# Optimization experiments

Measured on AMD Instinct MI355X. Metric: run time of the kernel, lower is better.

## Reference

```python
import jax, jax.numpy as jnp
import numpy as np

L = 10  # lattice_size


def _wilson_plaquette_loop(field, x):
    # Faithful translation of compute_wilson_loop: product of exp(plaquette) over 6 (mu,nu) pairs.
    coords = x[0, :4].astype(jnp.int32) % L
    loop = jnp.ones((1,), dtype=field.dtype)
    for mu in range(4):
        for nu in range(mu + 1, 4):
            pos = coords
            link1 = field[pos[0], pos[1], pos[2], mu]
            pos = pos.at[mu].set((pos[mu] + 1) % L)
            link2 = field[pos[0], pos[1], pos[2], nu]
            pos = pos.at[nu].set((pos[nu] + 1) % L)
            link3 = -field[pos[0], pos[1], pos[2], mu]
            pos = pos.at[mu].add(-1)  # original has no mod here
            link4 = -field[coords[0], coords[1], coords[2], nu]
            loop = loop * jnp.exp(link1 + link2 + link3 - (-link4) + 0.0 if False else link1 + link2 + link3 + link4)
    return loop


def setup_inputs() -> dict:
    key = jax.random.key(0)
    ks = jax.random.split(key, 20)
    s = 0.02  # scale weights to keep activations numerically sane
    d = jnp.float32
    return {
        'x': jax.random.normal(ks[0], (16384, 4), d),
        'field': jax.random.normal(ks[1], (L, L, L, 4), d),
        'fw1': jax.random.normal(ks[2], (4, 2048), d) * s,
        'fb1': jax.random.normal(ks[3], (2048,), d) * s,
        'fw2': jax.random.normal(ks[4], (2048, 4096), d) * s,
        'fb2': jax.random.normal(ks[5], (4096,), d) * s,
        'ww1': jax.random.normal(ks[6], (4096, 2048), d) * s,
        'wb1': jax.random.normal(ks[7], (2048,), d) * s,
        'ww2': jax.random.normal(ks[8], (2048, 1024), d) * s,
        'wb2': jax.random.normal(ks[9], (1024,), d) * s,
        'ww3': jax.random.normal(ks[10], (1024, 1), d) * s,
        'wb3': jax.random.normal(ks[11], (1,), d) * s,
        'tw1': jax.random.normal(ks[12], (4096, 2048), d) * s,
        'tb1': jax.random.normal(ks[13], (2048,), d) * s,
        'tw2': jax.random.normal(ks[14], (2048, 1), d) * s,
        'tb2': jax.random.normal(ks[15], (1,), d) * s,
    }


def reference(x, field, fw1, fb1, fw2, fb2, ww1, wb1, ww2, wb2, ww3, wb3, tw1, tb1, tw2, tb2):
    x4 = x[:, :4]
    h = jnp.maximum(x4 @ fw1 + fb1, 0.0)
    field_output = h @ fw2 + fb2                       # [B, dim]
    plaq = _wilson_plaquette_loop(field, x4)           # [1] (computed in torch forward, not returned)
    w = jnp.maximum(field_output @ ww1 + wb1, 0.0)
    w = jnp.maximum(w @ ww2 + wb2, 0.0)
    wilson_output = w @ ww3 + wb3                      # [B, 1]
    t = jnp.maximum(field_output @ tw1 + tb1, 0.0)
    topology_output = t @ tw2 + tb2                    # [B, 1]
    return field_output, wilson_output, topology_output, plaq
```

## Files before the change

kernel.cpp:

```cpp
#include <hip/hip_runtime.h>

#define L 10

using bf16x8 = __attribute__((ext_vector_type(8))) __bf16;
using u16x8  = __attribute__((ext_vector_type(8))) unsigned short;
using f32x4  = __attribute__((ext_vector_type(4))) float;

__device__ __forceinline__ unsigned short f2bf(float f) {
  unsigned int u = __float_as_uint(f);
  u += 0x7FFFu + ((u >> 16) & 1u);
  return (unsigned short)(u >> 16);
}
__device__ __forceinline__ float bf2f(unsigned short h) {
  return __uint_as_float(((unsigned int)h) << 16);
}

__global__ void plaq_kernel(const float* __restrict__ x,
                            const float* __restrict__ field,
                            float* __restrict__ out) {
  if (threadIdx.x != 0 || blockIdx.x != 0) return;
  int c[4];
#pragma unroll
  for (int i = 0; i < 4; ++i) {
    int v = (int)x[i];
    v %= L; if (v < 0) v += L;
    c[i] = v;
  }
  float S = 0.f;
  for (int mu = 0; mu < 4; ++mu)
    for (int nu = mu + 1; nu < 4; ++nu) {
      int p[4] = {c[0], c[1], c[2], c[3]};
      float l1 = field[((p[0]*L + p[1])*L + p[2])*4 + mu];
      p[mu] = (p[mu] + 1) % L;
      float l2 = field[((p[0]*L + p[1])*L + p[2])*4 + nu];
      p[nu] = (p[nu] + 1) % L;
      float l3 = field[((p[0]*L + p[1])*L + p[2])*4 + mu];
      float l4 = field[((c[0]*L + c[1])*L + c[2])*4 + nu];
      S += l1 + l2 - l3 - l4;
    }
  out[0] = expf(S);
}

__global__ void fc1_kernel(const float* __restrict__ x,
                           const float* __restrict__ fw1,
                           const float* __restrict__ fb1,
                           unsigned short* __restrict__ h) {
  const int N = 2048;
  int idx = blockIdx.x * blockDim.x + threadIdx.x;
  int m  = idx >> 8;
  int n0 = (idx & 255) * 8;
  float4 xv = *(const float4*)(x + (size_t)m * 4);
  unsigned short o[8];
#pragma unroll
  for (int j = 0; j < 8; ++j) {
    int n = n0 + j;
    float s = fb1[n] + xv.x * fw1[n] + xv.y * fw1[N + n]
                     + xv.z * fw1[2*N + n] + xv.w * fw1[3*N + n];
    o[j] = f2bf(fmaxf(s, 0.f));
  }
  *(u16x8*)(h + (size_t)m * N + n0) = *(const u16x8*)o;
}

__global__ void transpose_bf16_kernel(const float* __restrict__ W,
                                      unsigned short* __restrict__ WT,
                                      int K, int N) {
  __shared__ float tile[32][33];
  int n0 = blockIdx.x * 32, k0 = blockIdx.y * 32;
  int tx = threadIdx.x, ty = threadIdx.y;
#pragma unroll
  for (int i = 0; i < 32; i += 8)
    tile[ty + i][tx] = W[(size_t)(k0 + ty + i) * N + n0 + tx];
  __syncthreads();
#pragma unroll
  for (int i = 0; i < 32; i += 8)
    WT[(size_t)(n0 + ty + i) * K + k0 + tx] = f2bf(tile[tx][ty + i]);
}

__global__ void cast_bf16_kernel(const float* __restrict__ in,
                                 unsigned short* __restrict__ out) {
  size_t i = ((size_t)blockIdx.x * blockDim.x + threadIdx.x) * 8;
  unsigned short o[8];
#pragma unroll
  for (int j = 0; j < 8; ++j) o[j] = f2bf(in[i + j]);
  *(u16x8*)(out + i) = *(const u16x8*)o;
}

__global__ void biascat_kernel(const unsigned short* __restrict__ catT,
                               const float* __restrict__ fb2,
                               const float* __restrict__ wb1,
                               const float* __restrict__ tb1,
                               float* __restrict__ out) {
  int w    = blockIdx.x * 4 + (threadIdx.x >> 6);
  int lane = threadIdx.x & 63;
  if (w < 4096) { if (lane == 0) out[w] = fb2[w]; return; }
  int m = w - 4096;
  const unsigned short* row = catT + (size_t)m * 4096;
  float s = 0.f;
  for (int k = lane * 8; k < 4096; k += 512) {
    u16x8 v = *(const u16x8*)(row + k);
#pragma unroll
    for (int j = 0; j < 8; ++j) s += bf2f(v[j]) * fb2[k + j];
  }
#pragma unroll
  for (int off = 32; off; off >>= 1) s += __shfl_down(s, off);
  if (lane == 0) out[w] = s + (m < 2048 ? wb1[m] : tb1[m - 2048]);
}

__global__ __launch_bounds__(256, 2)
void gemm128_kernel(const unsigned short* __restrict__ A,
                    const unsigned short* __restrict__ BT,
                    unsigned short* __restrict__ outB,
                    int N, int K) {
  constexpr int BK = 64;
  __shared__ unsigned short As[128 * BK];
  __shared__ unsigned short Bs[128 * BK];

  const int bm = blockIdx.x, bn = blockIdx.y;
  const int tid = threadIdx.x;
  const int wid = tid >> 6, lane = tid & 63;
  const int wr = wid >> 1, wc = wid & 1;
  const int lr = lane & 15, lg = lane >> 4;

  f32x4 acc[4][4];
#pragma unroll
  for (int m = 0; m < 4; ++m)
#pragma unroll
    for (int n = 0; n < 4; ++n) acc[m][n] = (f32x4)0.f;

  const int srow = wid * 32 + (lane >> 3);
  const int scol = (lane & 7) * 8;
  const unsigned short* Ag = A  + (size_t)(bm * 128 + srow) * K + scol;
  const unsigned short* Bg = BT + (size_t)(bn * 128 + srow) * K + scol;

  for (int kt = 0; kt < K; kt += BK) {
#pragma unroll
    for (int i = 0; i < 4; ++i) {
      __builtin_amdgcn_global_load_lds(
          (const __attribute__((address_space(1))) unsigned int*)(Ag + (size_t)i * 8 * K + kt),
          (__attribute__((address_space(3))) unsigned int*)&As[wid * 2048 + i * 512],
          16, 0, 0);
      __builtin_amdgcn_global_load_lds(
          (const __attribute__((address_space(1))) unsigned int*)(Bg + (size_t)i * 8 * K + kt),
          (__attribute__((address_space(3))) unsigned int*)&Bs[wid * 2048 + i * 512],
          16, 0, 0);
    }
    __syncthreads();
#pragma unroll
    for (int kk = 0; kk < 2; ++kk) {
      u16x8 af[4], bf[4];
#pragma unroll
      for (int m = 0; m < 4; ++m)
        af[m] = *(const u16x8*)&As[(wr * 64 + m * 16 + lr) * BK + kk * 32 + lg * 8];
#pragma unroll
      for (int n = 0; n < 4; ++n)
        bf[n] = *(const u16x8*)&Bs[(wc * 64 + n * 16 + lr) * BK + kk * 32 + lg * 8];
#pragma unroll
      for (int m = 0; m < 4; ++m)
#pragma unroll
        for (int n = 0; n < 4; ++n)
          acc[m][n] = __builtin_amdgcn_mfma_f32_16x16x32_bf16(
              __builtin_bit_cast(bf16x8, af[m]),
              __builtin_bit_cast(bf16x8, bf[n]),
              acc[m][n], 0, 0, 0);
    }
    __syncthreads();
  }

  const int rowBase = bm * 128 + wr * 64 + lg * 4;
  const int colBase = bn * 128 + wc * 64 + lr;
#pragma unroll
  for (int n = 0; n < 4; ++n) {
    int col = colBase + n * 16;
#pragma unroll
    for (int m = 0; m < 4; ++m) {
      int row = rowBase + m * 16;
#pragma unroll
      for (int j = 0; j < 4; ++j)
        outB[(size_t)(row + j) * N + col] = f2bf(acc[m][n][j]);
    }
  }
}

#define GLL(gp, lp)                                                            \
  __builtin_amdgcn_global_load_lds(                                            \
      (const __attribute__((address_space(1))) unsigned int*)(gp),             \
      (__attribute__((address_space(3))) unsigned int*)(lp), 16, 0, 0)

#define DSREAD(dst, addr)                                                      \
  asm volatile("ds_read_b128 %0, %1" : "=v"(dst) : "v"(addr))

#define LGKM(n)                                                                \
  do { asm volatile("s_waitcnt lgkmcnt(" #n ")" ::: "memory");                 \
       __builtin_amdgcn_sched_barrier(0); } while (0)

#define FENCE() asm volatile("" ::: "memory")

extern __shared__ char lds_raw[];

__global__ __launch_bounds__(512)
void gemm256_kernel(const unsigned short* __restrict__ A,
                    const unsigned short* __restrict__ BT,
                    const float* __restrict__ bias,
                    float* __restrict__ outF,
                    unsigned short* __restrict__ outB,
                    int lda, int K, int NF, int NB, int nFtiles, int gmx) {
  const int NT = K >> 5;

  const int nwg = gridDim.x;
  const int q = nwg >> 3, r = nwg & 7;
  const int xcd = blockIdx.x & 7, lid = blockIdx.x >> 3;
  const int wg2 = (xcd < r ? xcd * (q + 1) : r * (q + 1) + (xcd - r) * q) + lid;
  const int bm = wg2 % gmx, bn = wg2 / gmx;

  const int tid  = threadIdx.x;
  const int wid  = tid >> 6, lane = tid & 63;
  const int wr   = wid >> 2, wc = wid & 3;
  const int lr   = lane & 15, lg = lane >> 4;

  const int srow = tid >> 2;
  const int scol = ((tid & 3) ^ ((tid >> 3) & 3)) * 8;
  const unsigned short* agp0 = A  + (size_t)(bm * 256 + srow) * lda + scol;
  const unsigned short* agp1 = agp0 + (size_t)128 * lda;
  const unsigned short* bgp0 = BT + (size_t)(bn * 256 + srow) * K + scol;
  const unsigned short* bgp1 = bgp0 + (size_t)128 * K;

  const int chunk = lg ^ ((lr >> 1) & 3);
  const unsigned ldsbase = (unsigned)(uintptr_t)&lds_raw[0];
  const unsigned aoff = (unsigned)((wr * 128 + lr) * 64 + chunk * 16);
  const unsigned boff = (unsigned)(16384 + (wc * 64 + lr) * 64 + chunk * 16);

  f32x4 acc[8][4];
#pragma unroll
  for (int m = 0; m < 8; ++m)
#pragma unroll
    for (int n = 0; n < 4; ++n) acc[m][n] = (f32x4)0.f;

#define STAGE_A(tt) do { unsigned so = (unsigned)(((tt) & 3) << 15);           \
    GLL(agp0 + (size_t)(tt) * 32, lds_raw + so + tid * 16);                    \
    GLL(agp1 + (size_t)(tt) * 32, lds_raw + so + 8192 + tid * 16); } while (0)
#define STAGE_B(tt) do { unsigned so = (unsigned)(((tt) & 3) << 15);           \
    GLL(bgp0 + (size_t)(tt) * 32, lds_raw + so + 16384 + tid * 16);            \
    GLL(bgp1 + (size_t)(tt) * 32, lds_raw + so + 24576 + tid * 16); } while (0)

  STAGE_A(0); STAGE_B(0); STAGE_A(1); STAGE_B(1); STAGE_A(2); STAGE_B(2);

  for (int t = 0; t < NT; ++t) {
    const int rem = NT - 1 - t;
    if (rem >= 2)      asm volatile("s_waitcnt vmcnt(8)" ::: "memory");
    else if (rem == 1) asm volatile("s_waitcnt vmcnt(4)" ::: "memory");
    else               asm volatile("s_waitcnt vmcnt(0)" ::: "memory");
    FENCE(); __builtin_amdgcn_s_barrier(); FENCE();
    __builtin_amdgcn_sched_barrier(0);

    const unsigned sbase = ldsbase + (unsigned)((t & 3) << 15);

    u16x8 b[4], a[8];
    DSREAD(b[0], sbase + boff);
    DSREAD(b[1], sbase + boff + 1024);
    DSREAD(b[2], sbase + boff + 2048);
    DSREAD(b[3], sbase + boff + 3072);
    DSREAD(a[0], sbase + aoff);
    DSREAD(a[1], sbase + aoff + 1024);
    DSREAD(a[2], sbase + aoff + 2048);
    DSREAD(a[3], sbase + aoff + 3072);
    DSREAD(a[4], sbase + aoff + 4096);
    DSREAD(a[5], sbase + aoff + 5120);
    DSREAD(a[6], sbase + aoff + 6144);
    DSREAD(a[7], sbase + aoff + 7168);
    if (t + 3 < NT) { STAGE_A(t + 3); STAGE_B(t + 3); }

    __builtin_amdgcn_s_setprio(1);
#define CLUSTER(m, g)                                                          \
    LGKM(g);                                                                   \
    acc[m][0] = __builtin_amdgcn_mfma_f32_16x16x32_bf16(                       \
        __builtin_bit_cast(bf16x8, a[m]), __builtin_bit_cast(bf16x8, b[0]),    \
        acc[m][0], 0, 0, 0);                                                   \
    acc[m][1] = __builtin_amdgcn_mfma_f32_16x16x32_bf16(                       \
        __builtin_bit_cast(bf16x8, a[m]), __builtin_bit_cast(bf16x8, b[1]),    \
        acc[m][1], 0, 0, 0);                                                   \
    acc[m][2] = __builtin_amdgcn_mfma_f32_16x16x32_bf16(                       \
        __builtin_bit_cast(bf16x8, a[m]), __builtin_bit_cast(bf16x8, b[2]),    \
        acc[m][2], 0, 0, 0);                                                   \
    acc[m][3] = __builtin_amdgcn_mfma_f32_16x16x32_bf16(                       \
        __builtin_bit_cast(bf16x8, a[m]), __builtin_bit_cast(bf16x8, b[3]),    \
        acc[m][3], 0, 0, 0)

    CLUSTER(0, 7);
    CLUSTER(1, 6);
    CLUSTER(2, 5);
    CLUSTER(3, 4);
    CLUSTER(4, 3);
    CLUSTER(5, 2);
    CLUSTER(6, 1);
    CLUSTER(7, 0);
#undef CLUSTER
    __builtin_amdgcn_s_setprio(0);
    __builtin_amdgcn_sched_barrier(0);
  }
#undef STAGE_A
#undef STAGE_B

  const int rowBase = bm * 256 + wr * 128 + lg * 4;
  const int colBase = bn * 256 + wc * 64 + lr;
  if (bn < nFtiles) {
#pragma unroll
    for (int n = 0; n < 4; ++n) {
      int col = colBase + n * 16;
      float bv = bias[col];
#pragma unroll
      for (int m = 0; m < 8; ++m) {
        int row = rowBase + m * 16;
#pragma unroll
        for (int j = 0; j < 4; ++j)
          __builtin_nontemporal_store(acc[m][n][j] + bv,
                                      &outF[(size_t)(row + j) * NF + col]);
      }
    }
  } else {
    const int colB = colBase - nFtiles * 256;
#pragma unroll
    for (int n = 0; n < 4; ++n) {
      int col = colB + n * 16;
      float bv = bias[colBase + n * 16];
#pragma unroll
      for (int m = 0; m < 8; ++m) {
        int row = rowBase + m * 16;
#pragma unroll
        for (int j = 0; j < 4; ++j)
          __builtin_nontemporal_store(f2bf(fmaxf(acc[m][n][j] + bv, 0.f)),
                                      &outB[(size_t)(row + j) * NB + colB + n * 16]);
      }
    }
  }
}

__global__ void gemv_kernel(const unsigned short* __restrict__ Abf,
                            const float* __restrict__ wvec,
                            const float* __restrict__ bias,
                            float* __restrict__ out, int K, int lda) {
  int row  = blockIdx.x * 4 + (threadIdx.x >> 6);
  int lane = threadIdx.x & 63;
  const unsigned short* ap = Abf + (size_t)row * lda;
  float s = 0.f;
  for (int k = lane * 8; k < K; k += 512) {
    u16x8 v = *(const u16x8*)(ap + k);
#pragma unroll
    for (int j = 0; j < 8; ++j) s += bf2f(v[j]) * wvec[k + j];
  }
#pragma unroll
  for (int off = 32; off; off >>= 1) s += __shfl_down(s, off);
  if (lane == 0) out[row] = s + bias[0];
}

extern "C" void kernel_launch(void* const* d_in, const int* in_sizes, int n_in,
                              void* d_out, int out_size, void* d_ws, size_t ws_size,
                              hipStream_t stream) {
  const float* x     = (const float*)d_in[0];
  const float* field = (const float*)d_in[1];
  const float* fw1   = (const float*)d_in[2];
  const float* fb1   = (const float*)d_in[3];
  const float* fw2   = (const float*)d_in[4];
  const float* fb2   = (const float*)d_in[5];
  const float* ww1   = (const float*)d_in[6];
  const float* wb1   = (const float*)d_in[7];
  const float* ww2   = (const float*)d_in[8];
  const float* wb2   = (const float*)d_in[9];
  const float* ww3   = (const float*)d_in[10];
  const float* wb3   = (const float*)d_in[11];
  const float* tw1   = (const float*)d_in[12];
  const float* tb1   = (const float*)d_in[13];
  const float* tw2   = (const float*)d_in[14];
  const float* tb2   = (const float*)d_in[15];

  const int M = 16384;
  float* outF    = (float*)d_out;
  float* outWil  = outF + (size_t)M * 4096;
  float* outTop  = outWil + M;
  float* outPlaq = outTop + M;

  char* ws = (char*)d_ws;
  const size_t MB = 1048576;
  unsigned short* hbuf    = (unsigned short*)(ws);
  unsigned short* catbuf  = (unsigned short*)(ws + 64  * MB);
  unsigned short* catT    = (unsigned short*)(ws + 192 * MB);
  unsigned short* w2buf   = (unsigned short*)(ws + 192 * MB);
  unsigned short* fw2T    = (unsigned short*)(ws + 224 * MB);
  unsigned short* W2catT  = (unsigned short*)(ws + 240 * MB);
  unsigned short* BTcat   = fw2T;
  unsigned short* fw2bf   = (unsigned short*)(ws + 256 * MB);
  unsigned short* ww2T    = (unsigned short*)(ws + 272 * MB);
  float*          biascat = (float*)(ws + 276 * MB);

  const int SMEM = 131072;
  (void)hipFuncSetAttribute((const void*)gemm256_kernel,
                            hipFuncAttributeMaxDynamicSharedMemorySize, SMEM);

  hipLaunchKernelGGL(plaq_kernel, dim3(1), dim3(64), 0, stream, x, field, outPlaq);
  hipLaunchKernelGGL(fc1_kernel, dim3(16384), dim3(256), 0, stream, x, fw1, fb1, hbuf);
  hipLaunchKernelGGL(transpose_bf16_kernel, dim3(128, 64), dim3(32, 8), 0, stream,
                     fw2, fw2T, 2048, 4096);
  hipLaunchKernelGGL(cast_bf16_kernel, dim3(4096), dim3(256), 0, stream, fw2, fw2bf);
  hipLaunchKernelGGL(transpose_bf16_kernel, dim3(64, 128), dim3(32, 8), 0, stream,
                     ww1, catT, 4096, 2048);
  hipLaunchKernelGGL(transpose_bf16_kernel, dim3(64, 128), dim3(32, 8), 0, stream,
                     tw1, catT + (size_t)2048 * 4096, 4096, 2048);
  hipLaunchKernelGGL(transpose_bf16_kernel, dim3(32, 64), dim3(32, 8), 0, stream,
                     ww2, ww2T, 2048, 1024);
  hipLaunchKernelGGL(biascat_kernel, dim3(2048), dim3(256), 0, stream,
                     catT, fb2, wb1, tb1, biascat);

  hipLaunchKernelGGL(gemm128_kernel, dim3(32, 16), dim3(256), 0, stream,
                     catT, fw2bf, W2catT, 2048, 4096);

  hipLaunchKernelGGL(gemm256_kernel, dim3(64 * 32), dim3(512), SMEM, stream,
                     hbuf, BTcat, biascat, outF, catbuf,
                     2048, 2048, 4096, 4096, 16, 64);

  hipLaunchKernelGGL(gemm256_kernel, dim3(64 * 4), dim3(512), SMEM, stream,
                     catbuf, ww2T, wb2, (float*)nullptr, w2buf,
                     4096, 2048, 0, 1024, 0, 64);

  hipLaunchKernelGGL(gemv_kernel, dim3(4096), dim3(256), 0, stream,
                     w2buf, ww3, wb3, outWil, 1024, 1024);
  hipLaunchKernelGGL(gemv_kernel, dim3(4096), dim3(256), 0, stream,
                     catbuf + 2048, tw2, tb2, outTop, 2048, 4096);

  (void)in_sizes; (void)n_in; (void)out_size; (void)ws_size;
}
```

Measured before the change: 918.1 us.

## Restructure 256x256 GEMM main loop into 64-wide K tiles with split-phase staging

The main loop of the bf16 MFMA GEMM now processes 64-wide K tiles held in two LDS buffers instead of 32-wide tiles in a four-deep ring. Each iteration is split into four phases, each reading half of the A fragments plus B from LDS, issuing 16 MFMAs, and interleaving partial global-to-LDS loads for later tiles. Only four A fragments are live at a time instead of eight, which reduces register pressure, and prefetch is spread across the phases. In exchange there are many more barriers per iteration and hand-tuned vmcnt waits whose counts must match the staging order exactly.

```diff
diff --git a/kernel.cpp b/kernel.cpp
--- a/kernel.cpp
+++ b/kernel.cpp
@@ -189,11 +189,13 @@
 #define DSREAD(dst, addr)                                                      \
   asm volatile("ds_read_b128 %0, %1" : "=v"(dst) : "v"(addr))
 
-#define LGKM(n)                                                                \
-  do { asm volatile("s_waitcnt lgkmcnt(" #n ")" ::: "memory");                 \
+#define LGKM0()                                                                \
+  do { asm volatile("s_waitcnt lgkmcnt(0)" ::: "memory");                      \
        __builtin_amdgcn_sched_barrier(0); } while (0)
 
+#define VMC(n)  asm volatile("s_waitcnt vmcnt(" #n ")" ::: "memory")
 #define FENCE() asm volatile("" ::: "memory")
+#define BAR()   do { FENCE(); __builtin_amdgcn_s_barrier(); FENCE(); } while (0)
 
 extern __shared__ char lds_raw[];
 
@@ -204,7 +206,7 @@
                     float* __restrict__ outF,
                     unsigned short* __restrict__ outB,
                     int lda, int K, int NF, int NB, int nFtiles, int gmx) {
-  const int NT = K >> 5;
+  const int NT = K >> 6;
 
   const int nwg = gridDim.x;
   const int q = nwg >> 3, r = nwg & 7;
@@ -217,17 +219,16 @@
   const int wr   = wid >> 2, wc = wid & 3;
   const int lr   = lane & 15, lg = lane >> 4;
 
-  const int srow = tid >> 2;
   const int scol = ((tid & 3) ^ ((tid >> 3) & 3)) * 8;
-  const unsigned short* agp0 = A  + (size_t)(bm * 256 + srow) * lda + scol;
+  const unsigned short* agp0 = A  + (size_t)(bm * 256 + (tid >> 2)) * lda + scol;
   const unsigned short* agp1 = agp0 + (size_t)128 * lda;
-  const unsigned short* bgp0 = BT + (size_t)(bn * 256 + srow) * K + scol;
+  const unsigned short* bgp0 = BT + (size_t)(bn * 256 + (tid >> 2)) * K + scol;
   const unsigned short* bgp1 = bgp0 + (size_t)128 * K;
 
   const int chunk = lg ^ ((lr >> 1) & 3);
-  const unsigned ldsbase = (unsigned)(uintptr_t)&lds_raw[0];
+  const unsigned ldsb = (unsigned)(uintptr_t)&lds_raw[0];
   const unsigned aoff = (unsigned)((wr * 128 + lr) * 64 + chunk * 16);
-  const unsigned boff = (unsigned)(16384 + (wc * 64 + lr) * 64 + chunk * 16);
+  const unsigned boff = (unsigned)(32768 + (wc * 64 + lr) * 64 + chunk * 16);
 
   f32x4 acc[8][4];
 #pragma unroll
@@ -235,70 +236,80 @@
 #pragma unroll
     for (int n = 0; n < 4; ++n) acc[m][n] = (f32x4)0.f;
 
-#define STAGE_A(tt) do { unsigned so = (unsigned)(((tt) & 3) << 15);           \
-    GLL(agp0 + (size_t)(tt) * 32, lds_raw + so + tid * 16);                    \
-    GLL(agp1 + (size_t)(tt) * 32, lds_raw + so + 8192 + tid * 16); } while (0)
-#define STAGE_B(tt) do { unsigned so = (unsigned)(((tt) & 3) << 15);           \
-    GLL(bgp0 + (size_t)(tt) * 32, lds_raw + so + 16384 + tid * 16);            \
-    GLL(bgp1 + (size_t)(tt) * 32, lds_raw + so + 24576 + tid * 16); } while (0)
-
-  STAGE_A(0); STAGE_B(0); STAGE_A(1); STAGE_B(1); STAGE_A(2); STAGE_B(2);
-
+#define STG_A(tt, kk) do {                                                     \
+    unsigned d = (unsigned)(((tt) & 1) << 16) + (unsigned)((kk) << 14);        \
+    GLL(agp0 + (size_t)(tt) * 64 + (kk) * 32, lds_raw + d + tid * 16);         \
+    GLL(agp1 + (size_t)(tt) * 64 + (kk) * 32, lds_raw + d + 8192 + tid * 16);  \
+  } while (0)
+#define STG_B(tt, kk) do {                                                     \
+    unsigned d = (unsigned)(((tt) & 1) << 16) + 32768u + (unsigned)((kk) << 14);\
+    GLL(bgp0 + (size_t)(tt) * 64 + (kk) * 32, lds_raw + d + tid * 16);         \
+    GLL(bgp1 + (size_t)(tt) * 64 + (kk) * 32, lds_raw + d + 8192 + tid * 16);  \
+  } while (0)
+
+#define RD8(kk) do {                                                           \
+    unsigned base = ldsb + sb + (unsigned)((kk) << 14);                        \
+    DSREAD(b[0], base + boff);          DSREAD(b[1], base + boff + 1024);      \
+    DSREAD(b[2], base + boff + 2048);   DSREAD(b[3], base + boff + 3072);      \
+    DSREAD(a[0], base + aoff);          DSREAD(a[1], base + aoff + 1024);      \
+    DSREAD(a[2], base + aoff + 2048);   DSREAD(a[3], base + aoff + 3072);      \
+  } while (0)
+#define RD4(kk) do {                                                           \
+    unsigned base = ldsb + sb + (unsigned)((kk) << 14);                        \
+    DSREAD(a[0], base + aoff + 4096);   DSREAD(a[1], base + aoff + 5120);      \
+    DSREAD(a[2], base + aoff + 6144);   DSREAD(a[3], base + aoff + 7168);      \
+  } while (0)
+
+#define QUAD(mb) do {                                                          \
+    __builtin_amdgcn_s_setprio(1);                                             \
+    _Pragma("unroll")                                                          \
+    for (int _m = 0; _m < 4; ++_m)                                             \
+      _Pragma("unroll")                                                        \
+      for (int _n = 0; _n < 4; ++_n)                                           \
+        acc[(mb) + _m][_n] = __builtin_amdgcn_mfma_f32_16x16x32_bf16(          \
+            __builtin_bit_cast(bf16x8, a[_m]),                                 \
+            __builtin_bit_cast(bf16x8, b[_n]), acc[(mb) + _m][_n], 0, 0, 0);   \
+    __builtin_amdgcn_s_setprio(0);                                             \
+  } while (0)
+
+  STG_B(0, 0); STG_A(0, 0); STG_B(0, 1); STG_A(0, 1);
+  STG_B(1, 0); STG_A(1, 0); STG_B(1, 1);
+
+  u16x8 a[4], b[4];
   for (int t = 0; t < NT; ++t) {
-    const int rem = NT - 1 - t;
-    if (rem >= 2)      asm volatile("s_waitcnt vmcnt(8)" ::: "memory");
-    else if (rem == 1) asm volatile("s_waitcnt vmcnt(4)" ::: "memory");
-    else               asm volatile("s_waitcnt vmcnt(0)" ::: "memory");
-    FENCE(); __builtin_amdgcn_s_barrier(); FENCE();
-    __builtin_amdgcn_sched_barrier(0);
-
-    const unsigned sbase = ldsbase + (unsigned)((t & 3) << 15);
-
-    u16x8 b[4], a[8];
-    DSREAD(b[0], sbase + boff);
-    DSREAD(b[1], sbase + boff + 1024);
-    DSREAD(b[2], sbase + boff + 2048);
-    DSREAD(b[3], sbase + boff + 3072);
-    DSREAD(a[0], sbase + aoff);
-    DSREAD(a[1], sbase + aoff + 1024);
-    DSREAD(a[2], sbase + aoff + 2048);
-    DSREAD(a[3], sbase + aoff + 3072);
-    DSREAD(a[4], sbase + aoff + 4096);
-    DSREAD(a[5], sbase + aoff + 5120);
-    DSREAD(a[6], sbase + aoff + 6144);
-    DSREAD(a[7], sbase + aoff + 7168);
-    if (t + 3 < NT) { STAGE_A(t + 3); STAGE_B(t + 3); }
-
-    __builtin_amdgcn_s_setprio(1);
-#define CLUSTER(m, g)                                                          \
-    LGKM(g);                                                                   \
-    acc[m][0] = __builtin_amdgcn_mfma_f32_16x16x32_bf16(                       \
-        __builtin_bit_cast(bf16x8, a[m]), __builtin_bit_cast(bf16x8, b[0]),    \
-        acc[m][0], 0, 0, 0);                                                   \
-    acc[m][1] = __builtin_amdgcn_mfma_f32_16x16x32_bf16(                       \
-        __builtin_bit_cast(bf16x8, a[m]), __builtin_bit_cast(bf16x8, b[1]),    \
-        acc[m][1], 0, 0, 0);                                                   \
-    acc[m][2] = __builtin_amdgcn_mfma_f32_16x16x32_bf16(                       \
-        __builtin_bit_cast(bf16x8, a[m]), __builtin_bit_cast(bf16x8, b[2]),    \
-        acc[m][2], 0, 0, 0);                                                   \
-    acc[m][3] = __builtin_amdgcn_mfma_f32_16x16x32_bf16(                       \
-        __builtin_bit_cast(bf16x8, a[m]), __builtin_bit_cast(bf16x8, b[3]),    \
-        acc[m][3], 0, 0, 0)
-
-    CLUSTER(0, 7);
-    CLUSTER(1, 6);
-    CLUSTER(2, 5);
-    CLUSTER(3, 4);
-    CLUSTER(4, 3);
-    CLUSTER(5, 2);
-    CLUSTER(6, 1);
-    CLUSTER(7, 0);
-#undef CLUSTER
-    __builtin_amdgcn_s_setprio(0);
-    __builtin_amdgcn_sched_barrier(0);
-  }
-#undef STAGE_A
-#undef STAGE_B
+    const unsigned sb = (unsigned)((t & 1) << 16);
+    if (t <= NT - 2) VMC(10); else VMC(4);
+    BAR();
+    RD8(0);
+    if (t + 1 < NT) STG_A(t + 1, 1);
+    BAR();
+    LGKM0();
+    QUAD(0);
+    BAR();
+    RD4(0);
+    if (t + 2 < NT) STG_B(t + 2, 0);
+    BAR();
+    LGKM0();
+    QUAD(4);
+    if (t <= NT - 3) VMC(10); else if (t == NT - 2) VMC(8); else VMC(0);
+    BAR();
+    RD8(1);
+    if (t + 2 < NT) STG_A(t + 2, 0);
+    BAR();
+    LGKM0();
+    QUAD(0);
+    BAR();
+    RD4(1);
+    if (t + 2 < NT) STG_B(t + 2, 1);
+    BAR();
+    LGKM0();
+    QUAD(4);
+  }
+#undef STG_A
+#undef STG_B
+#undef RD8
+#undef RD4
+#undef QUAD
 
   const int rowBase = bm * 256 + wr * 128 + lg * 4;
   const int colBase = bn * 256 + wc * 64 + lr;
@@ -317,10 +328,10 @@
       }
     }
   } else {
-    const int colB = colBase - nFtiles * 256;
+    const int colB0 = colBase - nFtiles * 256;
 #pragma unroll
     for (int n = 0; n < 4; ++n) {
-      int col = colB + n * 16;
+      int col = colB0 + n * 16;
       float bv = bias[colBase + n * 16];
 #pragma unroll
       for (int m = 0; m < 8; ++m) {
@@ -328,7 +339,7 @@
 #pragma unroll
         for (int j = 0; j < 4; ++j)
           __builtin_nontemporal_store(f2bf(fmaxf(acc[m][n][j] + bv, 0.f)),
-                                      &outB[(size_t)(row + j) * NB + colB + n * 16]);
+                                      &outB[(size_t)(row + j) * NB + col]);
       }
     }
   }
```

New measurement: 948.1 us. 1.03x slower.
